# Optimization experiments

Hardware: AMD Instinct MI355X
Metric: run time of the kernel (lower is better)

The kernel has to match this reference:

```python
import jax, jax.numpy as jnp
import numpy as np

B, C, H, W = 32, 32, 64, 64   # batch, in_channel, image height/width
HC = 1                        # hashtable channel groups (in_channel % HC == 0)
KS = 9                        # kernel_size: top-k neighbors per pixel
K = 64                        # kernel_number_per_pixel (output channels)
P = H * W                     # pixel_number


def setup_inputs() -> dict:
    key = jax.random.key(0)
    k1, k2, k3 = jax.random.split(key, 3)
    x = jax.random.normal(k1, (B, C, H, W), dtype=jnp.float32)
    # Per-pixel affinity scores -> top-KS neighbor indices (mimics
    # _build_full_hash: argsort descending, take first kernel_size).
    scores = jax.random.normal(k2, (HC, H, W, P), dtype=jnp.float32)
    idx = jnp.argsort(-scores, axis=-1)[..., :KS].astype(jnp.int32)  # (HC, NH, NW, KS)
    bound = float(np.sqrt(1.0 / (C * KS)))
    weights = jax.random.uniform(k3, (K, C * KS), minval=-bound, maxval=bound,
                                 dtype=jnp.float32)
    return {"x": x, "weights": weights, "idx": idx}


def reference(x, weights, idx):
    Bx, Cx, Hx, Wx = x.shape
    HCx, NH, NW, ks = idx.shape
    Px = Hx * Wx
    # full_hash[b, c, i, j, k] = idx[c % HC, i, j, k] + c*P + b*C*P,
    # so x.take(full_hash) == gather of x[b, c] at idx[c % HC].
    idx_full = jnp.tile(idx, (Cx // HCx, 1, 1, 1)).reshape(Cx, NH * NW * ks)
    g = jnp.take_along_axis(x.reshape(Bx, Cx, Px), idx_full[None], axis=2)  # (B, C, NH*NW*ks)
    # permute(1,4,0,2,3).reshape(C*ks, B*NH*NW)
    g = g.reshape(Bx, Cx, NH, NW, ks).transpose(1, 4, 0, 2, 3).reshape(Cx * ks, Bx * NH * NW)
    out = (weights @ g).reshape(-1, Bx, NH, NW)  # (K, B, NH, NW)
    return jnp.transpose(out, (1, 0, 2, 3))       # (B, K, NH, NW)
```

## Files before the change

kernel.cpp:

```cpp
#include <hip/hip_runtime.h>
#include <hip/hip_bf16.h>

#define BB 32
#define CC 32
#define PP 4096
#define KS 9
#define KK 64
#define CK 288

typedef __attribute__((ext_vector_type(8))) short short8;
typedef __attribute__((ext_vector_type(4))) float float4v;

__device__ inline unsigned short f2bf(float f) {
    __hip_bfloat16 h = __float2bfloat16(f);
    return __builtin_bit_cast(unsigned short, h);
}

__global__ __launch_bounds__(256)
void prep_kernel(const float* __restrict__ x, const float* __restrict__ w,
                 unsigned short* __restrict__ xt, unsigned short* __restrict__ wa) {
    const int t = threadIdx.x;
    const int blk = blockIdx.x;
    if (blk < 512) {
        const int b = blk >> 4;
        const int p = ((blk & 15) << 8) + t;
        const float* xb = x + (size_t)b * CC * PP + p;
        unsigned int buf[16];
#pragma unroll
        for (int c2 = 0; c2 < 16; ++c2) {
            float lo = xb[(size_t)(2 * c2) * PP];
            float hi = xb[(size_t)(2 * c2 + 1) * PP];
            buf[c2] = (unsigned int)f2bf(lo) | ((unsigned int)f2bf(hi) << 16);
        }
        uint4* dst = (uint4*)(xt + ((size_t)b * PP + p) * CC);
        const uint4* s = (const uint4*)buf;
#pragma unroll
        for (int j = 0; j < 4; ++j) dst[j] = s[j];
    } else {
        int i = (blk - 512) * 256 + t;
        if (i < KK * CK) {
            int j  = i & 7;
            int l  = (i >> 3) & 63;
            int mt = (i >> 9) & 3;
            int kc = i >> 11;
            int c  = ((l >> 4) << 3) + j;
            int ko = (mt << 4) + (l & 15);
            wa[i] = f2bf(w[ko * CK + c * KS + kc]);
        }
    }
}

__global__ __launch_bounds__(256, 4)
void abc_mfma3_kernel(const unsigned short* __restrict__ xt,
                      const unsigned short* __restrict__ wa,
                      const int* __restrict__ idx,
                      float* __restrict__ out) {
    __shared__ unsigned short was[KK * CK];
    const int t    = threadIdx.x;
    const int l    = t & 63;
    const int w    = t >> 6;
    const int blk  = blockIdx.x;
    const int b    = ((blk & 7) << 2) | ((blk >> 3) & 3);
    const int tile = blk >> 5;
    const int p0   = (tile << 7) + (w << 5);
    const int lo16 = l & 15;
    const int quad = l >> 4;

    {
        const uint4* s = (const uint4*)wa;
        uint4* d = (uint4*)was;
#pragma unroll
        for (int j = 0; j < 9; ++j) d[t + 256 * j] = s[t + 256 * j];
    }

    const unsigned short* xtb = xt + (size_t)b * PP * CC;

    int q[2][KS];
#pragma unroll
    for (int nt = 0; nt < 2; ++nt) {
        const int pl = p0 + nt * 16 + lo16;
#pragma unroll
        for (int kc = 0; kc < KS; ++kc) q[nt][kc] = idx[pl * KS + kc];
    }

    float4v acc[8];
#pragma unroll
    for (int i = 0; i < 8; ++i) acc[i] = (float4v){0.f, 0.f, 0.f, 0.f};

    __syncthreads();

    short8 bf[2][2];
#pragma unroll
    for (int nt = 0; nt < 2; ++nt)
        bf[0][nt] = *(const short8*)(xtb + (size_t)q[nt][0] * CC + (quad << 3));

#pragma unroll
    for (int kc = 0; kc < KS; ++kc) {
        const int cur = kc & 1, nxt = cur ^ 1;
        if (kc + 1 < KS) {
#pragma unroll
            for (int nt = 0; nt < 2; ++nt)
                bf[nxt][nt] = *(const short8*)(xtb + (size_t)q[nt][kc + 1] * CC + (quad << 3));
        }
#pragma unroll
        for (int mt = 0; mt < 4; ++mt) {
            const short8 a = *(const short8*)(was + ((size_t)(kc * 4 + mt) * 64 + l) * 8);
#pragma unroll
            for (int nt = 0; nt < 2; ++nt)
                acc[mt * 2 + nt] =
                    __builtin_amdgcn_mfma_f32_16x16x32_bf16(a, bf[cur][nt], acc[mt * 2 + nt], 0, 0, 0);
        }
    }

    float* ob = out + (size_t)b * KK * PP + p0 + lo16;
#pragma unroll
    for (int mt = 0; mt < 4; ++mt) {
        float* om = ob + (size_t)(mt * 16 + quad * 4) * PP;
#pragma unroll
        for (int r = 0; r < 4; ++r)
#pragma unroll
            for (int nt = 0; nt < 2; ++nt)
                __builtin_nontemporal_store(acc[mt * 2 + nt][r],
                                            om + (size_t)r * PP + nt * 16);
    }
}

__global__ __launch_bounds__(256)
void abc_valu_kernel(const float* __restrict__ x, const float* __restrict__ w,
                     const int* __restrict__ idx, float* __restrict__ out) {
    __shared__ float xrow[PP];
    const int t = threadIdx.x;
    const int b = blockIdx.x >> 4;
    const int p = ((blockIdx.x & 15) << 8) + t;
    int q[KS];
#pragma unroll
    for (int k = 0; k < KS; ++k) q[k] = idx[p * KS + k];
    float acc[KK];
#pragma unroll
    for (int i = 0; i < KK; ++i) acc[i] = 0.0f;
    const float* xb = x + (size_t)b * CC * PP;
#pragma unroll 1
    for (int c = 0; c < CC; ++c) {
        const float4* src = (const float4*)(xb + (size_t)c * PP);
        float4* dst = (float4*)xrow;
#pragma unroll
        for (int j = 0; j < 4; ++j) dst[j * 256 + t] = src[j * 256 + t];
        __syncthreads();
        float xv[KS];
#pragma unroll
        for (int k = 0; k < KS; ++k) xv[k] = xrow[q[k]];
#pragma unroll
        for (int k = 0; k < KS; ++k) {
            const int col = c * KS + k;
#pragma unroll
            for (int ko = 0; ko < KK; ++ko)
                acc[ko] += xv[k] * w[ko * CK + col];
        }
        __syncthreads();
    }
    float* ob = out + (size_t)b * KK * PP + p;
#pragma unroll
    for (int ko = 0; ko < KK; ++ko)
        ob[(size_t)ko * PP] = acc[ko];
}

extern "C" void kernel_launch(void* const* d_in, const int* in_sizes, int n_in,
                              void* d_out, int out_size, void* d_ws, size_t ws_size,
                              hipStream_t stream) {
    const float* x  = (const float*)d_in[0];
    const float* w  = (const float*)d_in[1];
    const int* idx  = (const int*)d_in[2];
    float* out      = (float*)d_out;

    const size_t xt_bytes = (size_t)BB * PP * CC * 2;
    const size_t need     = xt_bytes + (size_t)KK * CK * 2;

    if (ws_size >= need) {
        unsigned short* xt = (unsigned short*)d_ws;
        unsigned short* wa = (unsigned short*)((char*)d_ws + xt_bytes);
        const int wb_blocks = (KK * CK + 255) / 256;
        prep_kernel<<<512 + wb_blocks, 256, 0, stream>>>(x, w, xt, wa);
        abc_mfma3_kernel<<<BB * (PP / 128), 256, 0, stream>>>(xt, wa, idx, out);
    } else {
        abc_valu_kernel<<<BB * (PP / 256), 256, 0, stream>>>(x, w, idx, out);
    }
}
```

Baseline: 87.15 us.

## Switch gather-GEMM to 32x32x16 MFMA with triple-buffered gather prefetch

Replaces the 16x16x32 bf16 MFMA tiling (4 M-tiles by 2 N-tiles) with 32x32x16 MFMA (2 M-tiles by 2 K-halves), re-laying out the prepared weights to match. Each lane now gathers channel halves for a single pixel, and the gather prefetch deepens from double to triple buffering so loads run two kernel positions ahead. The aim is fewer MFMA instructions and index loads per wave and better latency hiding for the random gathers. In exchange each lane issues more scattered output stores and holds more registers.

```diff
diff --git a/kernel.cpp b/kernel.cpp
--- a/kernel.cpp
+++ b/kernel.cpp
@@ -9,7 +9,7 @@
 #define CK 288
 
 typedef __attribute__((ext_vector_type(8))) short short8;
-typedef __attribute__((ext_vector_type(4))) float float4v;
+typedef __attribute__((ext_vector_type(16))) float f32x16;
 
 __device__ inline unsigned short f2bf(float f) {
     __hip_bfloat16 h = __float2bfloat16(f);
@@ -41,17 +41,18 @@
         if (i < KK * CK) {
             int j  = i & 7;
             int l  = (i >> 3) & 63;
-            int mt = (i >> 9) & 3;
+            int mt = (i >> 9) & 1;
+            int kh = (i >> 10) & 1;
             int kc = i >> 11;
-            int c  = ((l >> 4) << 3) + j;
-            int ko = (mt << 4) + (l & 15);
+            int ko = (mt << 5) + (l & 31);
+            int c  = (kh << 4) + ((l >> 5) << 3) + j;
             wa[i] = f2bf(w[ko * CK + c * KS + kc]);
         }
     }
 }
 
 __global__ __launch_bounds__(256, 4)
-void abc_mfma3_kernel(const unsigned short* __restrict__ xt,
+void abc_mfma5_kernel(const unsigned short* __restrict__ xt,
                       const unsigned short* __restrict__ wa,
                       const int* __restrict__ idx,
                       float* __restrict__ out) {
@@ -63,8 +64,8 @@
     const int b    = ((blk & 7) << 2) | ((blk >> 3) & 3);
     const int tile = blk >> 5;
     const int p0   = (tile << 7) + (w << 5);
-    const int lo16 = l & 15;
-    const int quad = l >> 4;
+    const int gpix  = l & 31;
+    const int ghalf = l >> 5;
 
     {
         const uint4* s = (const uint4*)wa;
@@ -75,54 +76,54 @@
 
     const unsigned short* xtb = xt + (size_t)b * PP * CC;
 
-    int q[2][KS];
+    int q[KS];
+    {
+        const int* ip = idx + (size_t)(p0 + gpix) * KS;
 #pragma unroll
-    for (int nt = 0; nt < 2; ++nt) {
-        const int pl = p0 + nt * 16 + lo16;
-#pragma unroll
-        for (int kc = 0; kc < KS; ++kc) q[nt][kc] = idx[pl * KS + kc];
+        for (int kc = 0; kc < KS; ++kc) q[kc] = ip[kc];
     }
 
-    float4v acc[8];
+    f32x16 acc[2];
 #pragma unroll
-    for (int i = 0; i < 8; ++i) acc[i] = (float4v){0.f, 0.f, 0.f, 0.f};
+    for (int i = 0; i < 16; ++i) { acc[0][i] = 0.f; acc[1][i] = 0.f; }
 
     __syncthreads();
 
-    short8 bf[2][2];
+    short8 g[3][2];
 #pragma unroll
-    for (int nt = 0; nt < 2; ++nt)
-        bf[0][nt] = *(const short8*)(xtb + (size_t)q[nt][0] * CC + (quad << 3));
+    for (int kk = 0; kk < 2; ++kk)
+#pragma unroll
+        for (int kh = 0; kh < 2; ++kh)
+            g[kk][kh] = *(const short8*)(xtb + (size_t)q[kk] * CC + (kh << 4) + (ghalf << 3));
 
 #pragma unroll
     for (int kc = 0; kc < KS; ++kc) {
-        const int cur = kc & 1, nxt = cur ^ 1;
-        if (kc + 1 < KS) {
+        if (kc + 2 < KS) {
+            const int nb = (kc + 2) % 3;
 #pragma unroll
-            for (int nt = 0; nt < 2; ++nt)
-                bf[nxt][nt] = *(const short8*)(xtb + (size_t)q[nt][kc + 1] * CC + (quad << 3));
+            for (int kh = 0; kh < 2; ++kh)
+                g[nb][kh] = *(const short8*)(xtb + (size_t)q[kc + 2] * CC + (kh << 4) + (ghalf << 3));
         }
+        const int cb = kc % 3;
 #pragma unroll
-        for (int mt = 0; mt < 4; ++mt) {
-            const short8 a = *(const short8*)(was + ((size_t)(kc * 4 + mt) * 64 + l) * 8);
+        for (int mt = 0; mt < 2; ++mt) {
 #pragma unroll
-            for (int nt = 0; nt < 2; ++nt)
-                acc[mt * 2 + nt] =
-                    __builtin_amdgcn_mfma_f32_16x16x32_bf16(a, bf[cur][nt], acc[mt * 2 + nt], 0, 0, 0);
+            for (int kh = 0; kh < 2; ++kh) {
+                const short8 a =
+                    *(const short8*)(was + ((size_t)(((kc * 2 + kh) * 2 + mt) * 64 + l)) * 8);
+                acc[mt] = __builtin_amdgcn_mfma_f32_32x32x16_bf16(a, g[cb][kh], acc[mt], 0, 0, 0);
+            }
         }
     }
 
-    float* ob = out + (size_t)b * KK * PP + p0 + lo16;
+    float* ob = out + (size_t)b * KK * PP + p0 + gpix;
 #pragma unroll
-    for (int mt = 0; mt < 4; ++mt) {
-        float* om = ob + (size_t)(mt * 16 + quad * 4) * PP;
+    for (int mt = 0; mt < 2; ++mt)
 #pragma unroll
-        for (int r = 0; r < 4; ++r)
-#pragma unroll
-            for (int nt = 0; nt < 2; ++nt)
-                __builtin_nontemporal_store(acc[mt * 2 + nt][r],
-                                            om + (size_t)r * PP + nt * 16);
-    }
+        for (int r = 0; r < 16; ++r) {
+            const int row = (mt << 5) + (r & 3) + ((r >> 2) << 3) + (ghalf << 2);
+            __builtin_nontemporal_store(acc[mt][r], ob + (size_t)row * PP);
+        }
 }
 
 __global__ __launch_bounds__(256)
@@ -180,7 +181,7 @@
         unsigned short* wa = (unsigned short*)((char*)d_ws + xt_bytes);
         const int wb_blocks = (KK * CK + 255) / 256;
         prep_kernel<<<512 + wb_blocks, 256, 0, stream>>>(x, w, xt, wa);
-        abc_mfma3_kernel<<<BB * (PP / 128), 256, 0, stream>>>(xt, wa, idx, out);
+        abc_mfma5_kernel<<<BB * (PP / 128), 256, 0, stream>>>(xt, wa, idx, out);
     } else {
         abc_valu_kernel<<<BB * (PP / 256), 256, 0, stream>>>(x, w, idx, out);
     }
```

Result: no change. 88.57 us (+1.6%).
